# Kernel optimization log

Measured on AMD Instinct MI355X. Metric: run time of the kernel, lower is better.

The kernel has to match this reference:

```python
import jax, jax.numpy as jnp
import numpy as np


def _pairwise_sqdist(x, y):
    # x: [B, Nx, D] (gts), y: [B, Ny, D] (preds)
    # P[b,i,j] = ||x[b,i]||^2 + ||y[b,j]||^2 - 2 <x[b,i], y[b,j]>
    rx = jnp.sum(x * x, axis=-1)  # [B, Nx]
    ry = jnp.sum(y * y, axis=-1)  # [B, Ny]
    zz = jnp.einsum('bid,bjd->bij', x, y)  # [B, Nx, Ny]
    return rx[:, :, None] + ry[:, None, :] - 2.0 * zz


def setup_inputs() -> dict:
    key = jax.random.key(0)
    k1, k2 = jax.random.split(key)
    B, N, D = 8, 8192, 3
    preds = jax.random.normal(k1, (B, N, D), dtype=jnp.float32)
    gts = jax.random.normal(k2, (B, N, D), dtype=jnp.float32)
    return {"preds": preds, "gts": gts}


def reference(preds, gts):
    # Original: P = batch_pairwise_dist(gts, preds) -> [B, N_gts, N_preds]
    P = _pairwise_sqdist(gts, preds)
    loss_1 = jnp.sum(jnp.min(P, axis=1))  # min over gts points, per pred point
    loss_2 = jnp.sum(jnp.min(P, axis=2))  # min over pred points, per gt point
    return loss_1 + loss_2
```

## Files before the change

### kernel.cpp

```cpp
#include <hip/hip_runtime.h>

#define NPTS   8192
#define NBATCH 8
#define BLKT   256
#define CHUNK  2048
#define NCHUNK (NPTS / CHUNK)

typedef __attribute__((ext_vector_type(8)))  short bf16x8;
typedef __attribute__((ext_vector_type(16))) float f32x16;

__device__ __forceinline__ void bsplit(float v, unsigned int& h, unsigned int& l) {
    unsigned int u = __float_as_uint(v);
    h = u >> 16;
    float rem = v - __uint_as_float(u & 0xFFFF0000u);
    l = __float_as_uint(rem) >> 16;
}


__global__ __launch_bounds__(BLKT, 2) void chamfer_r7(
    const float* __restrict__ preds,
    const float* __restrict__ gts,
    float* __restrict__ out)
{
    __shared__ uint4 lds4[(CHUNK * 16 + 256 * 16) / 8];
    __shared__ float wsum[4];
    unsigned short* lds = (unsigned short*)lds4;

    const int tid  = threadIdx.x;
    const int wave = tid >> 6;
    const int lane = tid & 63;
    const int n    = lane & 31;
    const int h    = lane >> 5;

    const int rchunk = blockIdx.x;
    const int batch  = blockIdx.y;
    const int dir    = blockIdx.z;

    const float* rows = ((dir == 0) ? gts   : preds) + (size_t)batch * NPTS * 3;
    const float* cols = ((dir == 0) ? preds : gts)   + (size_t)batch * NPTS * 3;
    const int ibase = rchunk * 256;
    const unsigned int ONE = 0x3F80u;

    const int B_LO = 0;
    const int B_HI = CHUNK * 8;
    const int A_LO = CHUNK * 16;
    const int A_HI = CHUNK * 16 + 2048;

    {
        int gi = ibase + tid;
        float x = rows[gi * 3 + 0], y = rows[gi * 3 + 1], z = rows[gi * 3 + 2];
        float g2 = x * x + y * y + z * z;
        unsigned int xh, xl, yh, yl, zh, zl, gh, gl;
        bsplit(x, xh, xl); bsplit(y, yh, yl); bsplit(z, zh, zl); bsplit(g2, gh, gl);
        ((uint4*)(lds + A_LO))[tid] = make_uint4(xh | (yh << 16), zh | (gh << 16),
                                                 ONE | (xh << 16), yh | (zh << 16));
        ((uint4*)(lds + A_HI))[tid] = make_uint4(gh | (ONE << 16), xl | (yl << 16),
                                                 zl | (gl << 16), 0u);
    }
    __syncthreads();

    bf16x8 afr[2];
    #pragma unroll
    for (int t = 0; t < 2; ++t) {
        int row = wave * 64 + t * 32 + n;
        afr[t] = *(const bf16x8*)&lds[(h ? A_HI : A_LO) + row * 8];
    }
    f32x16 rmin[2];
    #pragma unroll
    for (int t = 0; t < 2; ++t)
        #pragma unroll
        for (int e = 0; e < 16; ++e) rmin[t][e] = 3.4e38f;
    __syncthreads();

    const f32x16 zeroC = (f32x16)(0.f);

    for (int ch = 0; ch < NCHUNK; ++ch) {
        #pragma unroll
        for (int j = 0; j < CHUNK / BLKT; ++j) {
            int c  = j * BLKT + tid;
            int gc = ch * CHUNK + c;
            float x = cols[gc * 3 + 0], y = cols[gc * 3 + 1], z = cols[gc * 3 + 2];
            float p2 = x * x + y * y + z * z;
            unsigned int cxh, cxl, cyh, cyl, czh, czl, ph, pl;
            bsplit(-2.f * x, cxh, cxl); bsplit(-2.f * y, cyh, cyl);
            bsplit(-2.f * z, czh, czl); bsplit(p2, ph, pl);
            ((uint4*)(lds + B_LO))[c] = make_uint4(cxh | (cyh << 16), czh | (ONE << 16),
                                                   ph | (cxl << 16), cyl | (czl << 16));
            ((uint4*)(lds + B_HI))[c] = make_uint4(pl << 16, cxh | (cyh << 16),
                                                   czh | (ONE << 16), ph);
        }
        __syncthreads();

        const unsigned short* bp = &lds[(h ? B_HI : B_LO) + n * 8];

        #pragma unroll 8
        for (int jt2 = 0; jt2 < CHUNK / 64; ++jt2) {
            bf16x8 b0 = *(const bf16x8*)(bp + (jt2 * 2 + 0) * 256);
            bf16x8 b1 = *(const bf16x8*)(bp + (jt2 * 2 + 1) * 256);
            f32x16 c0a = __builtin_amdgcn_mfma_f32_32x32x16_bf16(afr[0], b0, zeroC, 0, 0, 0);
            f32x16 c0b = __builtin_amdgcn_mfma_f32_32x32x16_bf16(afr[0], b1, zeroC, 0, 0, 0);
            f32x16 c1a = __builtin_amdgcn_mfma_f32_32x32x16_bf16(afr[1], b0, zeroC, 0, 0, 0);
            f32x16 c1b = __builtin_amdgcn_mfma_f32_32x32x16_bf16(afr[1], b1, zeroC, 0, 0, 0);
            #pragma unroll
            for (int e = 0; e < 16; ++e) {
                rmin[0][e] = fminf(fminf(c0a[e], c0b[e]), rmin[0][e]);
                rmin[1][e] = fminf(fminf(c1a[e], c1b[e]), rmin[1][e]);
            }
        }
        __syncthreads();
    }

    float s = 0.f;
    #pragma unroll
    for (int t = 0; t < 2; ++t) {
        #pragma unroll
        for (int e = 0; e < 16; ++e) {
            float v = rmin[t][e];
            v = fminf(v, __shfl_xor(v, 1, 64));
            v = fminf(v, __shfl_xor(v, 2, 64));
            v = fminf(v, __shfl_xor(v, 4, 64));
            v = fminf(v, __shfl_xor(v, 8, 64));
            v = fminf(v, __shfl_xor(v, 16, 64));
            if (n == 0) s += v;
        }
    }
    #pragma unroll
    for (int off = 32; off > 0; off >>= 1)
        s += __shfl_down(s, off, 64);
    if (lane == 0) wsum[wave] = s;
    __syncthreads();
    if (tid == 0)
        atomicAdd(out, wsum[0] + wsum[1] + wsum[2] + wsum[3]);
}

extern "C" void kernel_launch(void* const* d_in, const int* in_sizes, int n_in,
                              void* d_out, int out_size, void* d_ws, size_t ws_size,
                              hipStream_t stream) {
    const float* preds = (const float*)d_in[0];
    const float* gts   = (const float*)d_in[1];
    float* out = (float*)d_out;

    dim3 grid(NPTS / 256, NBATCH, 2);
    chamfer_r7<<<grid, dim3(BLKT), 0, stream>>>(preds, gts, out);
}
```

Measured before the change: 92.46 us.

## Precompute split-bf16 column fragments in a prep kernel and register-prefetch chunks

Adds a prep kernel that converts every point once into its hi/lo bf16 MFMA B-fragment layout and stores it in the workspace. The main kernel then streams these preformatted uint4 chunks, prefetching the next chunk into registers while MFMAs run on the current one. This replaces the per-block recomputation of column encodings, which every row-block previously redid for all 8192 points. It also halves the LDS chunk so more blocks can be resident, at the cost of an extra launch, workspace traffic and more synchronisation rounds. A fallback kernel keeps the old path when the workspace is too small.

```diff
diff --git a/kernel.cpp b/kernel.cpp
--- a/kernel.cpp
+++ b/kernel.cpp
@@ -3,8 +3,9 @@
 #define NPTS   8192
 #define NBATCH 8
 #define BLKT   256
-#define CHUNK  2048
+#define CHUNK  1024
 #define NCHUNK (NPTS / CHUNK)
+#define CVEC   (CHUNK * 2 / BLKT)
 
 typedef __attribute__((ext_vector_type(8)))  short bf16x8;
 typedef __attribute__((ext_vector_type(16))) float f32x16;
@@ -17,14 +18,42 @@
 }
 
 
-__global__ __launch_bounds__(BLKT, 2) void chamfer_r7(
+__global__ __launch_bounds__(BLKT) void prep_ext(
     const float* __restrict__ preds,
     const float* __restrict__ gts,
+    uint4* __restrict__ extbuf)
+{
+    const unsigned int ONE = 0x3F80u;
+    int g   = blockIdx.x * BLKT + threadIdx.x;
+    int set = g >> 16;
+    int idx = g & 65535;
+    int j   = idx & 8191;
+
+    const float* src = (set == 0) ? preds : gts;
+    float x = src[idx * 3 + 0], y = src[idx * 3 + 1], z = src[idx * 3 + 2];
+    float p2 = x * x + y * y + z * z;
+    unsigned int cxh, cxl, cyh, cyl, czh, czl, ph, pl;
+    bsplit(-2.f * x, cxh, cxl); bsplit(-2.f * y, cyh, cyl);
+    bsplit(-2.f * z, czh, czl); bsplit(p2, ph, pl);
+
+    uint4* dst = extbuf + (size_t)set * 131072 + (idx >> 13) * 16384
+               + (j >> 5) * 64 + (j & 31);
+    dst[0]  = make_uint4(cxh | (cyh << 16), czh | (ONE << 16),
+                         ph | (cxl << 16), cyl | (czl << 16));
+    dst[32] = make_uint4(pl << 16, cxh | (cyh << 16),
+                         czh | (ONE << 16), ph);
+}
+
+__global__ __launch_bounds__(BLKT, 2) void chamfer_r8(
+    const float* __restrict__ preds,
+    const float* __restrict__ gts,
+    const uint4* __restrict__ extbuf,
     float* __restrict__ out)
 {
-    __shared__ uint4 lds4[(CHUNK * 16 + 256 * 16) / 8];
+    __shared__ uint4 lds4[2560];
     __shared__ float wsum[4];
     unsigned short* lds = (unsigned short*)lds4;
+    const int A_LO = 16384, A_HI = 18432;
 
     const int tid  = threadIdx.x;
     const int wave = tid >> 6;
@@ -36,19 +65,119 @@
     const int batch  = blockIdx.y;
     const int dir    = blockIdx.z;
 
+    const float* rows = ((dir == 0) ? gts : preds) + (size_t)batch * NPTS * 3;
+    const uint4* gb   = extbuf + (size_t)((dir == 0) ? 0 : 1) * 131072
+                      + (size_t)batch * 16384;
+    const int ibase = rchunk * 256;
+    const unsigned int ONE = 0x3F80u;
+
+    uint4 R[CVEC];
+    #pragma unroll
+    for (int p = 0; p < CVEC; ++p) R[p] = gb[p * BLKT + tid];
+
+    {
+        int gi = ibase + tid;
+        float x = rows[gi * 3 + 0], y = rows[gi * 3 + 1], z = rows[gi * 3 + 2];
+        float g2 = x * x + y * y + z * z;
+        unsigned int xh, xl, yh, yl, zh, zl, gh, gl;
+        bsplit(x, xh, xl); bsplit(y, yh, yl); bsplit(z, zh, zl); bsplit(g2, gh, gl);
+        lds4[2048 + tid] = make_uint4(xh | (yh << 16), zh | (gh << 16),
+                                      ONE | (xh << 16), yh | (zh << 16));
+        lds4[2304 + tid] = make_uint4(gh | (ONE << 16), xl | (yl << 16),
+                                      zl | (gl << 16), 0u);
+    }
+    __syncthreads();
+
+    bf16x8 afr[2];
+    #pragma unroll
+    for (int t = 0; t < 2; ++t) {
+        int row = wave * 64 + t * 32 + n;
+        afr[t] = *(const bf16x8*)&lds[(h ? A_HI : A_LO) + row * 8];
+    }
+    f32x16 rmin[2];
+    #pragma unroll
+    for (int t = 0; t < 2; ++t)
+        #pragma unroll
+        for (int e = 0; e < 16; ++e) rmin[t][e] = 3.4e38f;
+
+    const f32x16 zeroC = (f32x16)(0.f);
+    const unsigned short* bp = &lds[lane * 8];
+
+    for (int ch = 0; ch < NCHUNK; ++ch) {
+        #pragma unroll
+        for (int p = 0; p < CVEC; ++p) lds4[p * BLKT + tid] = R[p];
+        __syncthreads();
+
+        if (ch < NCHUNK - 1) {
+            #pragma unroll
+            for (int p = 0; p < CVEC; ++p)
+                R[p] = gb[(ch + 1) * 2048 + p * BLKT + tid];
+        }
+
+        #pragma unroll 4
+        for (int jt2 = 0; jt2 < CHUNK / 64; ++jt2) {
+            bf16x8 b0 = *(const bf16x8*)(bp + jt2 * 1024);
+            bf16x8 b1 = *(const bf16x8*)(bp + jt2 * 1024 + 512);
+            f32x16 c0a = __builtin_amdgcn_mfma_f32_32x32x16_bf16(afr[0], b0, zeroC, 0, 0, 0);
+            f32x16 c0b = __builtin_amdgcn_mfma_f32_32x32x16_bf16(afr[0], b1, zeroC, 0, 0, 0);
+            f32x16 c1a = __builtin_amdgcn_mfma_f32_32x32x16_bf16(afr[1], b0, zeroC, 0, 0, 0);
+            f32x16 c1b = __builtin_amdgcn_mfma_f32_32x32x16_bf16(afr[1], b1, zeroC, 0, 0, 0);
+            #pragma unroll
+            for (int e = 0; e < 16; ++e) {
+                rmin[0][e] = fminf(fminf(c0a[e], c0b[e]), rmin[0][e]);
+                rmin[1][e] = fminf(fminf(c1a[e], c1b[e]), rmin[1][e]);
+            }
+        }
+        __syncthreads();
+    }
+
+    float s = 0.f;
+    #pragma unroll
+    for (int t = 0; t < 2; ++t) {
+        #pragma unroll
+        for (int e = 0; e < 16; ++e) {
+            float v = rmin[t][e];
+            v = fminf(v, __shfl_xor(v, 1, 64));
+            v = fminf(v, __shfl_xor(v, 2, 64));
+            v = fminf(v, __shfl_xor(v, 4, 64));
+            v = fminf(v, __shfl_xor(v, 8, 64));
+            v = fminf(v, __shfl_xor(v, 16, 64));
+            if (n == 0) s += v;
+        }
+    }
+    #pragma unroll
+    for (int off = 32; off > 0; off >>= 1)
+        s += __shfl_down(s, off, 64);
+    if (lane == 0) wsum[wave] = s;
+    __syncthreads();
+    if (tid == 0)
+        atomicAdd(out, wsum[0] + wsum[1] + wsum[2] + wsum[3]);
+}
+
+__global__ __launch_bounds__(BLKT, 2) void chamfer_fb(
+    const float* __restrict__ preds,
+    const float* __restrict__ gts,
+    float* __restrict__ out)
+{
+    __shared__ uint4 ldsf4[(2048 * 16 + 256 * 16) / 8];
+    __shared__ float wsum[4];
+    unsigned short* lds = (unsigned short*)ldsf4;
+
+    const int tid  = threadIdx.x;
+    const int wave = tid >> 6;
+    const int lane = tid & 63;
+    const int n    = lane & 31;
+    const int h    = lane >> 5;
+    const int rchunk = blockIdx.x, batch = blockIdx.y, dir = blockIdx.z;
     const float* rows = ((dir == 0) ? gts   : preds) + (size_t)batch * NPTS * 3;
     const float* cols = ((dir == 0) ? preds : gts)   + (size_t)batch * NPTS * 3;
     const int ibase = rchunk * 256;
     const unsigned int ONE = 0x3F80u;
-
-    const int B_LO = 0;
-    const int B_HI = CHUNK * 8;
-    const int A_LO = CHUNK * 16;
-    const int A_HI = CHUNK * 16 + 2048;
+    const int B_LO = 0, B_HI = 2048 * 8, A_LO = 2048 * 16, A_HI = 2048 * 16 + 2048;
 
     {
         int gi = ibase + tid;
-        float x = rows[gi * 3 + 0], y = rows[gi * 3 + 1], z = rows[gi * 3 + 2];
+        float x = rows[gi * 3], y = rows[gi * 3 + 1], z = rows[gi * 3 + 2];
         float g2 = x * x + y * y + z * z;
         unsigned int xh, xl, yh, yl, zh, zl, gh, gl;
         bsplit(x, xh, xl); bsplit(y, yh, yl); bsplit(z, zh, zl); bsplit(g2, gh, gl);
@@ -58,28 +187,22 @@
                                                  zl | (gl << 16), 0u);
     }
     __syncthreads();
-
     bf16x8 afr[2];
     #pragma unroll
-    for (int t = 0; t < 2; ++t) {
-        int row = wave * 64 + t * 32 + n;
-        afr[t] = *(const bf16x8*)&lds[(h ? A_HI : A_LO) + row * 8];
-    }
+    for (int t = 0; t < 2; ++t)
+        afr[t] = *(const bf16x8*)&lds[(h ? A_HI : A_LO) + (wave * 64 + t * 32 + n) * 8];
     f32x16 rmin[2];
     #pragma unroll
     for (int t = 0; t < 2; ++t)
         #pragma unroll
         for (int e = 0; e < 16; ++e) rmin[t][e] = 3.4e38f;
     __syncthreads();
-
     const f32x16 zeroC = (f32x16)(0.f);
-
-    for (int ch = 0; ch < NCHUNK; ++ch) {
-        #pragma unroll
-        for (int j = 0; j < CHUNK / BLKT; ++j) {
-            int c  = j * BLKT + tid;
-            int gc = ch * CHUNK + c;
-            float x = cols[gc * 3 + 0], y = cols[gc * 3 + 1], z = cols[gc * 3 + 2];
+    for (int ch = 0; ch < 4; ++ch) {
+        #pragma unroll
+        for (int j = 0; j < 8; ++j) {
+            int c = j * BLKT + tid, gc = ch * 2048 + c;
+            float x = cols[gc * 3], y = cols[gc * 3 + 1], z = cols[gc * 3 + 2];
             float p2 = x * x + y * y + z * z;
             unsigned int cxh, cxl, cyh, cyl, czh, czl, ph, pl;
             bsplit(-2.f * x, cxh, cxl); bsplit(-2.f * y, cyh, cyl);
@@ -90,11 +213,9 @@
                                                    czh | (ONE << 16), ph);
         }
         __syncthreads();
-
         const unsigned short* bp = &lds[(h ? B_HI : B_LO) + n * 8];
-
         #pragma unroll 8
-        for (int jt2 = 0; jt2 < CHUNK / 64; ++jt2) {
+        for (int jt2 = 0; jt2 < 32; ++jt2) {
             bf16x8 b0 = *(const bf16x8*)(bp + (jt2 * 2 + 0) * 256);
             bf16x8 b1 = *(const bf16x8*)(bp + (jt2 * 2 + 1) * 256);
             f32x16 c0a = __builtin_amdgcn_mfma_f32_32x32x16_bf16(afr[0], b0, zeroC, 0, 0, 0);
@@ -109,10 +230,9 @@
         }
         __syncthreads();
     }
-
     float s = 0.f;
     #pragma unroll
-    for (int t = 0; t < 2; ++t) {
+    for (int t = 0; t < 2; ++t)
         #pragma unroll
         for (int e = 0; e < 16; ++e) {
             float v = rmin[t][e];
@@ -123,14 +243,11 @@
             v = fminf(v, __shfl_xor(v, 16, 64));
             if (n == 0) s += v;
         }
-    }
-    #pragma unroll
-    for (int off = 32; off > 0; off >>= 1)
-        s += __shfl_down(s, off, 64);
+    #pragma unroll
+    for (int off = 32; off > 0; off >>= 1) s += __shfl_down(s, off, 64);
     if (lane == 0) wsum[wave] = s;
     __syncthreads();
-    if (tid == 0)
-        atomicAdd(out, wsum[0] + wsum[1] + wsum[2] + wsum[3]);
+    if (tid == 0) atomicAdd(out, wsum[0] + wsum[1] + wsum[2] + wsum[3]);
 }
 
 extern "C" void kernel_launch(void* const* d_in, const int* in_sizes, int n_in,
@@ -141,5 +258,12 @@
     float* out = (float*)d_out;
 
     dim3 grid(NPTS / 256, NBATCH, 2);
-    chamfer_r7<<<grid, dim3(BLKT), 0, stream>>>(preds, gts, out);
-}
+
+    if (ws_size >= (size_t)4 * 1024 * 1024) {
+        uint4* extbuf = (uint4*)d_ws;
+        prep_ext<<<dim3(512), dim3(BLKT), 0, stream>>>(preds, gts, extbuf);
+        chamfer_r8<<<grid, dim3(BLKT), 0, stream>>>(preds, gts, extbuf, out);
+    } else {
+        chamfer_fb<<<grid, dim3(BLKT), 0, stream>>>(preds, gts, out);
+    }
+}
```

New measurement: 113.7 us. +22.9%, slower.

## Split column chunk across two wave groups and prefetch next chunk into registers

Applied to the files above, without the earlier changes.

Doubles the block to 512 threads: eight waves, where four row groups each take half of the column chunk, and a final LDS pass combines the two partial minima per row. Global loads of the next column chunk are issued into registers before the MFMA loop so they overlap with compute instead of stalling the LDS fill. The aim is more waves in flight to hide latency and fewer exposed global loads. In exchange it adds register pressure under the tighter launch bound, plus an extra LDS reduction and barrier.

```diff
diff --git a/kernel.cpp b/kernel.cpp
--- a/kernel.cpp
+++ b/kernel.cpp
@@ -2,9 +2,10 @@
 
 #define NPTS   8192
 #define NBATCH 8
-#define BLKT   256
+#define BLKT   512
 #define CHUNK  2048
 #define NCHUNK (NPTS / CHUNK)
+#define CPT    (CHUNK / BLKT)
 
 typedef __attribute__((ext_vector_type(8)))  short bf16x8;
 typedef __attribute__((ext_vector_type(16))) float f32x16;
@@ -17,20 +18,22 @@
 }
 
 
-__global__ __launch_bounds__(BLKT, 2) void chamfer_r7(
+__global__ __launch_bounds__(BLKT, 4) void chamfer_r9(
     const float* __restrict__ preds,
     const float* __restrict__ gts,
     float* __restrict__ out)
 {
-    __shared__ uint4 lds4[(CHUNK * 16 + 256 * 16) / 8];
-    __shared__ float wsum[4];
+    __shared__ uint4 lds4[4608];
     unsigned short* lds = (unsigned short*)lds4;
+    float* fbuf = (float*)lds4;
 
     const int tid  = threadIdx.x;
     const int wave = tid >> 6;
     const int lane = tid & 63;
     const int n    = lane & 31;
     const int h    = lane >> 5;
+    const int rg   = wave & 3;
+    const int cf   = wave >> 2;
 
     const int rchunk = blockIdx.x;
     const int batch  = blockIdx.y;
@@ -40,29 +43,34 @@
     const float* cols = ((dir == 0) ? preds : gts)   + (size_t)batch * NPTS * 3;
     const int ibase = rchunk * 256;
     const unsigned int ONE = 0x3F80u;
+    const int B_HI = 16384, A_LO = 32768, A_HI = 34816;
 
-    const int B_LO = 0;
-    const int B_HI = CHUNK * 8;
-    const int A_LO = CHUNK * 16;
-    const int A_HI = CHUNK * 16 + 2048;
+    float R[3 * CPT];
+    #pragma unroll
+    for (int j = 0; j < CPT; ++j) {
+        int c = j * BLKT + tid;
+        R[j * 3 + 0] = cols[c * 3 + 0];
+        R[j * 3 + 1] = cols[c * 3 + 1];
+        R[j * 3 + 2] = cols[c * 3 + 2];
+    }
 
-    {
+    if (tid < 256) {
         int gi = ibase + tid;
         float x = rows[gi * 3 + 0], y = rows[gi * 3 + 1], z = rows[gi * 3 + 2];
         float g2 = x * x + y * y + z * z;
         unsigned int xh, xl, yh, yl, zh, zl, gh, gl;
         bsplit(x, xh, xl); bsplit(y, yh, yl); bsplit(z, zh, zl); bsplit(g2, gh, gl);
-        ((uint4*)(lds + A_LO))[tid] = make_uint4(xh | (yh << 16), zh | (gh << 16),
-                                                 ONE | (xh << 16), yh | (zh << 16));
-        ((uint4*)(lds + A_HI))[tid] = make_uint4(gh | (ONE << 16), xl | (yl << 16),
-                                                 zl | (gl << 16), 0u);
+        lds4[4096 + tid] = make_uint4(xh | (yh << 16), zh | (gh << 16),
+                                      ONE | (xh << 16), yh | (zh << 16));
+        lds4[4352 + tid] = make_uint4(gh | (ONE << 16), xl | (yl << 16),
+                                      zl | (gl << 16), 0u);
     }
     __syncthreads();
 
     bf16x8 afr[2];
     #pragma unroll
     for (int t = 0; t < 2; ++t) {
-        int row = wave * 64 + t * 32 + n;
+        int row = rg * 64 + t * 32 + n;
         afr[t] = *(const bf16x8*)&lds[(h ? A_HI : A_LO) + row * 8];
     }
     f32x16 rmin[2];
@@ -70,33 +78,40 @@
     for (int t = 0; t < 2; ++t)
         #pragma unroll
         for (int e = 0; e < 16; ++e) rmin[t][e] = 3.4e38f;
-    __syncthreads();
 
     const f32x16 zeroC = (f32x16)(0.f);
+    const unsigned short* bp = &lds[(h ? B_HI : 0) + (cf * 1024 + n) * 8];
 
     for (int ch = 0; ch < NCHUNK; ++ch) {
         #pragma unroll
-        for (int j = 0; j < CHUNK / BLKT; ++j) {
-            int c  = j * BLKT + tid;
-            int gc = ch * CHUNK + c;
-            float x = cols[gc * 3 + 0], y = cols[gc * 3 + 1], z = cols[gc * 3 + 2];
+        for (int j = 0; j < CPT; ++j) {
+            int c = j * BLKT + tid;
+            float x = R[j * 3 + 0], y = R[j * 3 + 1], z = R[j * 3 + 2];
             float p2 = x * x + y * y + z * z;
             unsigned int cxh, cxl, cyh, cyl, czh, czl, ph, pl;
             bsplit(-2.f * x, cxh, cxl); bsplit(-2.f * y, cyh, cyl);
             bsplit(-2.f * z, czh, czl); bsplit(p2, ph, pl);
-            ((uint4*)(lds + B_LO))[c] = make_uint4(cxh | (cyh << 16), czh | (ONE << 16),
-                                                   ph | (cxl << 16), cyl | (czl << 16));
-            ((uint4*)(lds + B_HI))[c] = make_uint4(pl << 16, cxh | (cyh << 16),
-                                                   czh | (ONE << 16), ph);
+            lds4[c]        = make_uint4(cxh | (cyh << 16), czh | (ONE << 16),
+                                        ph | (cxl << 16), cyl | (czl << 16));
+            lds4[2048 + c] = make_uint4(pl << 16, cxh | (cyh << 16),
+                                        czh | (ONE << 16), ph);
         }
         __syncthreads();
 
-        const unsigned short* bp = &lds[(h ? B_HI : B_LO) + n * 8];
+        if (ch < NCHUNK - 1) {
+            #pragma unroll
+            for (int j = 0; j < CPT; ++j) {
+                int c = (ch + 1) * CHUNK + j * BLKT + tid;
+                R[j * 3 + 0] = cols[c * 3 + 0];
+                R[j * 3 + 1] = cols[c * 3 + 1];
+                R[j * 3 + 2] = cols[c * 3 + 2];
+            }
+        }
 
-        #pragma unroll 8
-        for (int jt2 = 0; jt2 < CHUNK / 64; ++jt2) {
-            bf16x8 b0 = *(const bf16x8*)(bp + (jt2 * 2 + 0) * 256);
-            bf16x8 b1 = *(const bf16x8*)(bp + (jt2 * 2 + 1) * 256);
+        #pragma unroll 4
+        for (int jt2 = 0; jt2 < 16; ++jt2) {
+            bf16x8 b0 = *(const bf16x8*)(bp + jt2 * 512);
+            bf16x8 b1 = *(const bf16x8*)(bp + jt2 * 512 + 256);
             f32x16 c0a = __builtin_amdgcn_mfma_f32_32x32x16_bf16(afr[0], b0, zeroC, 0, 0, 0);
             f32x16 c0b = __builtin_amdgcn_mfma_f32_32x32x16_bf16(afr[0], b1, zeroC, 0, 0, 0);
             f32x16 c1a = __builtin_amdgcn_mfma_f32_32x32x16_bf16(afr[1], b0, zeroC, 0, 0, 0);
@@ -110,7 +125,6 @@
         __syncthreads();
     }
 
-    float s = 0.f;
     #pragma unroll
     for (int t = 0; t < 2; ++t) {
         #pragma unroll
@@ -121,16 +135,27 @@
             v = fminf(v, __shfl_xor(v, 4, 64));
             v = fminf(v, __shfl_xor(v, 8, 64));
             v = fminf(v, __shfl_xor(v, 16, 64));
-            if (n == 0) s += v;
+            if (n == 0) {
+                int row = rg * 64 + t * 32 + (e & 3) + 8 * (e >> 2) + 4 * h;
+                fbuf[cf * 256 + row] = v;
+            }
         }
     }
+    __syncthreads();
+
+    float s = 0.f;
+    if (tid < 256) s = fminf(fbuf[tid], fbuf[256 + tid]);
     #pragma unroll
     for (int off = 32; off > 0; off >>= 1)
         s += __shfl_down(s, off, 64);
-    if (lane == 0) wsum[wave] = s;
+    if (lane == 0) fbuf[512 + wave] = s;
     __syncthreads();
-    if (tid == 0)
-        atomicAdd(out, wsum[0] + wsum[1] + wsum[2] + wsum[3]);
+    if (tid == 0) {
+        float tot = 0.f;
+        #pragma unroll
+        for (int w = 0; w < 8; ++w) tot += fbuf[512 + w];
+        atomicAdd(out, tot);
+    }
 }
 
 extern "C" void kernel_launch(void* const* d_in, const int* in_sizes, int n_in,
@@ -141,5 +166,5 @@
     float* out = (float*)d_out;
 
     dim3 grid(NPTS / 256, NBATCH, 2);
-    chamfer_r7<<<grid, dim3(BLKT), 0, stream>>>(preds, gts, out);
+    chamfer_r9<<<grid, dim3(BLKT), 0, stream>>>(preds, gts, out);
 }
```

Result: slower. 125.6 us (+35.8%).
